# Optimization experiments

Measured on AMD Instinct MI355X. Metric: run time of the kernel, lower is better.

The kernel has to match this reference:

```python
import jax, jax.numpy as jnp
import numpy as np


def setup_inputs() -> dict:
    key = jax.random.key(0)
    k1, k2, k3 = jax.random.split(key, 3)
    B, N, C, H, W = 4, 6, 80, 16, 44
    image_features = jax.random.normal(k1, (B * N, C, H, W), dtype=jnp.float32)
    # eye + small perturbation keeps the 3x3 intrinsics block invertible
    intrinsics = jnp.eye(4, dtype=jnp.float32) + 0.1 * jax.random.normal(k2, (B, N, 4, 4), dtype=jnp.float32)
    extrinsics = jnp.eye(4, dtype=jnp.float32) + 0.1 * jax.random.normal(k3, (B, N, 4, 4), dtype=jnp.float32)
    return {"image_features": image_features, "intrinsics": intrinsics,
            "extrinsics": extrinsics, "depth_bins": 59}


def reference(image_features, intrinsics, extrinsics, depth_bins):
    BN, C, H, W = image_features.shape
    N = intrinsics.shape[1]
    B = BN // N
    dt = image_features.dtype
    depths = jnp.linspace(0.1, 1.0, depth_bins).astype(dt)  # (D,)
    feats = image_features.reshape(B, N, C, H, W)

    # pixel homogeneous coords, matching torch meshgrid(indexing='ij') + flatten
    yy, xx = jnp.meshgrid(jnp.arange(H), jnp.arange(W), indexing='ij')
    xy1 = jnp.stack([xx.ravel(), yy.ravel(), jnp.ones(H * W)], axis=0).astype(dt)  # (3, HW)

    K_inv = jnp.linalg.inv(intrinsics[:, :, :3, :3])            # (B,N,3,3)
    rays = jnp.einsum('bnij,jp->bnip', K_inv, xy1)              # (B,N,3,HW)

    # softmax over spatial dim (dim=3 of (B,N,C,HW) in the torch code)
    depth_probs = jax.nn.softmax(feats.reshape(B, N, C, H * W), axis=3)

    # In the original, only the LAST 4 channels of the (4C+1)-channel homogeneous
    # volume enter the extrinsic matmul: the [x,y,z] coords of channel C-1 plus 1.
    d_last = depth_probs[:, :, -1]                              # (B,N,HW)
    # (B,N,3,HW,D) = rays * (prob * depth)
    pts = rays[..., None] * (d_last[:, :, None, :, None] * depths)

    R = extrinsics[:, :, :3, :3]                                # (B,N,3,3)
    t = extrinsics[:, :, :3, 3]                                 # (B,N,3)
    world = jnp.einsum('bnij,bnjpd->bnipd', R, pts) + t[:, :, :, None, None]
    world = world.reshape(B, N, 3, H, W, depth_bins)

    feats_rep = jnp.broadcast_to(feats[..., None], (B, N, C, H, W, depth_bins))
    return jnp.concatenate([world, feats_rep], axis=2)         # (B,N,3+C,H,W,D)
```

## Files before the change

kernel.cpp:

```cpp
#include <hip/hip_runtime.h>


#define BB 4
#define NN 6
#define CC 80
#define HH 16
#define WW 44
#define DD 59
#define BN (BB*NN)
#define PP (HH*WW)
#define CHO (CC+3)
#define WD (WW*DD)
#define DSTEP (0.9f/58.f)
#define NF8 10342464u
#define SWEEPB 2048

typedef float fx4 __attribute__((ext_vector_type(4)));
typedef unsigned int uint;

__device__ inline float waveMax(float v) {
#pragma unroll
    for (int o = 32; o; o >>= 1) v = fmaxf(v, __shfl_xor(v, o));
    return v;
}
__device__ inline float waveSum(float v) {
#pragma unroll
    for (int o = 32; o; o >>= 1) v += __shfl_xor(v, o);
    return v;
}

__global__ __launch_bounds__(256) void lss_prep(const float* __restrict__ feats,
                                                const float* __restrict__ intr,
                                                const float* __restrict__ extr,
                                                float* __restrict__ Vw,
                                                float* __restrict__ Tarr) {
    const int bn = blockIdx.x;
    const int tid = threadIdx.x;
    __shared__ float sf[PP];
    __shared__ float sred[4];
    __shared__ float sbc[2];

    const float* f = feats + ((size_t)bn * CC + (CC - 1)) * PP;
    float m = -1e30f;
    for (int p = tid; p < PP; p += 256) { float v = f[p]; sf[p] = v; m = fmaxf(m, v); }
    m = waveMax(m);
    if ((tid & 63) == 0) sred[tid >> 6] = m;
    __syncthreads();
    if (tid == 0) sbc[0] = fmaxf(fmaxf(sred[0], sred[1]), fmaxf(sred[2], sred[3]));
    __syncthreads();
    const float mm = sbc[0];
    float s = 0.f;
    for (int p = tid; p < PP; p += 256) { float e = expf(sf[p] - mm); sf[p] = e; s += e; }
    s = waveSum(s);
    if ((tid & 63) == 0) sred[tid >> 6] = s;
    __syncthreads();
    if (tid == 0) sbc[1] = sred[0] + sred[1] + sred[2] + sred[3];
    __syncthreads();
    const float inv = 1.0f / sbc[1];

    const float* K = intr + bn * 16;
    float a = K[0], b = K[1], c = K[2];
    float d = K[4], e = K[5], ff = K[6];
    float g = K[8], h9 = K[9], i9 = K[10];
    float det = a * (e * i9 - ff * h9) - b * (d * i9 - ff * g) + c * (d * h9 - e * g);
    float id = 1.0f / det;
    float kinv[9] = {
        (e * i9 - ff * h9) * id, (c * h9 - b * i9) * id, (b * ff - c * e) * id,
        (ff * g - d * i9) * id,  (a * i9 - c * g) * id,  (c * d - a * ff) * id,
        (d * h9 - e * g) * id,   (b * g - a * h9) * id,  (a * e - b * d) * id
    };
    const float* E = extr + bn * 16;
#pragma unroll
    for (int ch = 0; ch < 3; ++ch) {
        float M0 = E[ch * 4 + 0] * kinv[0] + E[ch * 4 + 1] * kinv[3] + E[ch * 4 + 2] * kinv[6];
        float M1 = E[ch * 4 + 0] * kinv[1] + E[ch * 4 + 1] * kinv[4] + E[ch * 4 + 2] * kinv[7];
        float M2 = E[ch * 4 + 0] * kinv[2] + E[ch * 4 + 1] * kinv[5] + E[ch * 4 + 2] * kinv[8];
        float* vrow = Vw + (size_t)(bn * 3 + ch) * PP;
        for (int p = tid; p < PP; p += 256) {
            int hl = p / WW;
            int w  = p - hl * WW;
            float ray = M0 * (float)w + M1 * (float)hl + M2;
            vrow[p] = ray * sf[p] * inv;
        }
        if (tid == 0) Tarr[bn * 3 + ch] = E[ch * 4 + 3];
    }
}

__global__ __launch_bounds__(256) void lss_sweep(const float* __restrict__ feats,
                                                 const float* __restrict__ Vw,
                                                 const float* __restrict__ Tarr,
                                                 float* __restrict__ out) {
    const uint stride = gridDim.x * 256u;
    for (uint g = blockIdx.x * 256u + threadIdx.x; g < NF8; g += stride) {
        uint sl = g / 5192u;
        uint e8 = (g - sl * 5192u) << 3;
        uint p  = e8 / 59u;
        uint d0 = e8 - 59u * p;
        uint bn = sl / 83u;
        uint ch = sl - 83u * bn;
        uint kc = 59u - d0;
        uint cw = (kc < 8u) ? 1u : 0u;

        float vv[8];
        if (ch < 3u) {
            uint wrow = bn * 3u + ch;
            const float* src = Vw + wrow * (uint)PP;
            float T  = Tarr[wrow];
            float vA = src[p];
            float vB = src[p + cw];
#pragma unroll
            for (int k = 0; k < 8; ++k) {
                bool cr = ((uint)k >= kc);
                float val = cr ? vB : vA;
                uint dk = d0 + (uint)k - (cr ? 59u : 0u);
                vv[k] = val * (0.1f + (float)dk * DSTEP) + T;
            }
        } else {
            const float* src = feats + (bn * (uint)CC + (ch - 3u)) * (uint)PP;
            float vA = src[p];
            float vB = src[p + cw];
#pragma unroll
            for (int k = 0; k < 8; ++k) vv[k] = ((uint)k >= kc) ? vB : vA;
        }
        fx4 lo, hi;
        lo.x = vv[0]; lo.y = vv[1]; lo.z = vv[2]; lo.w = vv[3];
        hi.x = vv[4]; hi.y = vv[5]; hi.z = vv[6]; hi.w = vv[7];
        ((fx4*)out)[2u * g]      = lo;
        ((fx4*)out)[2u * g + 1u] = hi;
    }
}

extern "C" void kernel_launch(void* const* d_in, const int* in_sizes, int n_in,
                              void* d_out, int out_size, void* d_ws, size_t ws_size,
                              hipStream_t stream) {
    const float* feats = (const float*)d_in[0];
    const float* intr  = (const float*)d_in[1];
    const float* extr  = (const float*)d_in[2];
    float* out  = (float*)d_out;
    float* Vw   = (float*)d_ws;
    float* Tarr = (float*)d_ws + 50688 + 16;

    lss_prep<<<BN, 256, 0, stream>>>(feats, intr, extr, Vw, Tarr);
    lss_sweep<<<SWEEPB, 256, 0, stream>>>(feats, Vw, Tarr, out);
}
```

Before: 72.87 us.

## Fuse prep and sweep into one kernel with specialized world-coord and feature blocks

Result: faster. 66.06 us (-9.3%).

```diff
diff --git a/kernel.cpp b/kernel.cpp
--- a/kernel.cpp
+++ b/kernel.cpp
@@ -10,10 +10,12 @@
 #define BN (BB*NN)
 #define PP (HH*WW)
 #define CHO (CC+3)
-#define WD (WW*DD)
 #define DSTEP (0.9f/58.f)
-#define NF8 10342464u
-#define SWEEPB 2048
+#define Q4S 10384u
+#define NFS 1920u
+#define NFF4 (NFS*Q4S)
+#define WBLK 72
+#define FBLK 2048
 
 typedef float fx4 __attribute__((ext_vector_type(4)));
 typedef unsigned int uint;
@@ -29,104 +31,108 @@
     return v;
 }
 
-__global__ __launch_bounds__(256) void lss_prep(const float* __restrict__ feats,
-                                                const float* __restrict__ intr,
-                                                const float* __restrict__ extr,
-                                                float* __restrict__ Vw,
-                                                float* __restrict__ Tarr) {
-    const int bn = blockIdx.x;
+__global__ __launch_bounds__(256) void lss_fused(const float* __restrict__ feats,
+                                                 const float* __restrict__ intr,
+                                                 const float* __restrict__ extr,
+                                                 float* __restrict__ out) {
+    const int blk = blockIdx.x;
     const int tid = threadIdx.x;
+
     __shared__ float sf[PP];
+    __shared__ float vw[PP + 1];
     __shared__ float sred[4];
     __shared__ float sbc[2];
 
-    const float* f = feats + ((size_t)bn * CC + (CC - 1)) * PP;
-    float m = -1e30f;
-    for (int p = tid; p < PP; p += 256) { float v = f[p]; sf[p] = v; m = fmaxf(m, v); }
-    m = waveMax(m);
-    if ((tid & 63) == 0) sred[tid >> 6] = m;
-    __syncthreads();
-    if (tid == 0) sbc[0] = fmaxf(fmaxf(sred[0], sred[1]), fmaxf(sred[2], sred[3]));
-    __syncthreads();
-    const float mm = sbc[0];
-    float s = 0.f;
-    for (int p = tid; p < PP; p += 256) { float e = expf(sf[p] - mm); sf[p] = e; s += e; }
-    s = waveSum(s);
-    if ((tid & 63) == 0) sred[tid >> 6] = s;
-    __syncthreads();
-    if (tid == 0) sbc[1] = sred[0] + sred[1] + sred[2] + sred[3];
-    __syncthreads();
-    const float inv = 1.0f / sbc[1];
+    if (blk < WBLK) {
+        const int bn = blk / 3;
+        const int ch = blk - 3 * bn;
 
-    const float* K = intr + bn * 16;
-    float a = K[0], b = K[1], c = K[2];
-    float d = K[4], e = K[5], ff = K[6];
-    float g = K[8], h9 = K[9], i9 = K[10];
-    float det = a * (e * i9 - ff * h9) - b * (d * i9 - ff * g) + c * (d * h9 - e * g);
-    float id = 1.0f / det;
-    float kinv[9] = {
-        (e * i9 - ff * h9) * id, (c * h9 - b * i9) * id, (b * ff - c * e) * id,
-        (ff * g - d * i9) * id,  (a * i9 - c * g) * id,  (c * d - a * ff) * id,
-        (d * h9 - e * g) * id,   (b * g - a * h9) * id,  (a * e - b * d) * id
-    };
-    const float* E = extr + bn * 16;
-#pragma unroll
-    for (int ch = 0; ch < 3; ++ch) {
+        const float* f = feats + ((size_t)bn * CC + (CC - 1)) * PP;
+        float m = -1e30f;
+        for (int p = tid; p < PP; p += 256) { float v = f[p]; sf[p] = v; m = fmaxf(m, v); }
+        m = waveMax(m);
+        if ((tid & 63) == 0) sred[tid >> 6] = m;
+        __syncthreads();
+        if (tid == 0) sbc[0] = fmaxf(fmaxf(sred[0], sred[1]), fmaxf(sred[2], sred[3]));
+        __syncthreads();
+        const float mm = sbc[0];
+        float s = 0.f;
+        for (int p = tid; p < PP; p += 256) { float e = expf(sf[p] - mm); sf[p] = e; s += e; }
+        s = waveSum(s);
+        if ((tid & 63) == 0) sred[tid >> 6] = s;
+        __syncthreads();
+        if (tid == 0) sbc[1] = sred[0] + sred[1] + sred[2] + sred[3];
+        __syncthreads();
+        const float inv = 1.0f / sbc[1];
+
+        const float* K = intr + bn * 16;
+        float a = K[0], b = K[1], c = K[2];
+        float d = K[4], e = K[5], ff = K[6];
+        float g = K[8], h9 = K[9], i9 = K[10];
+        float det = a * (e * i9 - ff * h9) - b * (d * i9 - ff * g) + c * (d * h9 - e * g);
+        float id = 1.0f / det;
+        float kinv[9] = {
+            (e * i9 - ff * h9) * id, (c * h9 - b * i9) * id, (b * ff - c * e) * id,
+            (ff * g - d * i9) * id,  (a * i9 - c * g) * id,  (c * d - a * ff) * id,
+            (d * h9 - e * g) * id,   (b * g - a * h9) * id,  (a * e - b * d) * id
+        };
+        const float* E = extr + bn * 16;
         float M0 = E[ch * 4 + 0] * kinv[0] + E[ch * 4 + 1] * kinv[3] + E[ch * 4 + 2] * kinv[6];
         float M1 = E[ch * 4 + 0] * kinv[1] + E[ch * 4 + 1] * kinv[4] + E[ch * 4 + 2] * kinv[7];
         float M2 = E[ch * 4 + 0] * kinv[2] + E[ch * 4 + 1] * kinv[5] + E[ch * 4 + 2] * kinv[8];
-        float* vrow = Vw + (size_t)(bn * 3 + ch) * PP;
+        const float T = E[ch * 4 + 3];
+
         for (int p = tid; p < PP; p += 256) {
             int hl = p / WW;
             int w  = p - hl * WW;
             float ray = M0 * (float)w + M1 * (float)hl + M2;
-            vrow[p] = ray * sf[p] * inv;
+            vw[p] = ray * sf[p] * inv;
         }
-        if (tid == 0) Tarr[bn * 3 + ch] = E[ch * 4 + 3];
-    }
-}
+        if (tid == 0) vw[PP] = 0.f;
+        __syncthreads();
 
-__global__ __launch_bounds__(256) void lss_sweep(const float* __restrict__ feats,
-                                                 const float* __restrict__ Vw,
-                                                 const float* __restrict__ Tarr,
-                                                 float* __restrict__ out) {
-    const uint stride = gridDim.x * 256u;
-    for (uint g = blockIdx.x * 256u + threadIdx.x; g < NF8; g += stride) {
-        uint sl = g / 5192u;
-        uint e8 = (g - sl * 5192u) << 3;
-        uint p  = e8 / 59u;
-        uint d0 = e8 - 59u * p;
-        uint bn = sl / 83u;
-        uint ch = sl - 83u * bn;
-        uint kc = 59u - d0;
-        uint cw = (kc < 8u) ? 1u : 0u;
-
-        float vv[8];
-        if (ch < 3u) {
-            uint wrow = bn * 3u + ch;
-            const float* src = Vw + wrow * (uint)PP;
-            float T  = Tarr[wrow];
-            float vA = src[p];
-            float vB = src[p + cw];
+        const uint s0 = (uint)(bn * CHO + ch) * Q4S;
+        for (uint q = tid; q < Q4S; q += 256u) {
+            uint c4 = q << 2;
+            uint p  = c4 / 59u;
+            uint d0 = c4 - 59u * p;
+            uint kc = 59u - d0;
+            uint cw = (kc < 4u) ? 1u : 0u;
+            float vA = vw[p];
+            float vB = vw[p + cw];
+            fx4 r;
 #pragma unroll
-            for (int k = 0; k < 8; ++k) {
+            for (int k = 0; k < 4; ++k) {
                 bool cr = ((uint)k >= kc);
                 float val = cr ? vB : vA;
                 uint dk = d0 + (uint)k - (cr ? 59u : 0u);
-                vv[k] = val * (0.1f + (float)dk * DSTEP) + T;
+                r[k] = val * (0.1f + (float)dk * DSTEP) + T;
             }
-        } else {
-            const float* src = feats + (bn * (uint)CC + (ch - 3u)) * (uint)PP;
+            ((fx4*)out)[s0 + q] = r;
+        }
+    } else {
+        const uint stride = FBLK * 256u;
+        for (uint g = (uint)(blk - WBLK) * 256u + tid; g < NFF4; g += stride) {
+            uint fs = g / Q4S;
+            uint r4 = g - fs * Q4S;
+            uint c4 = r4 << 2;
+            uint p  = c4 / 59u;
+            uint d0 = c4 - 59u * p;
+            uint bn = fs / 80u;
+            uint chf = fs - 80u * bn;
+            uint kc = 59u - d0;
+            uint cw = (kc < 4u) ? 1u : 0u;
+
+            const float* src = feats + ((size_t)bn * CC + chf) * PP;
             float vA = src[p];
             float vB = src[p + cw];
+            fx4 r;
 #pragma unroll
-            for (int k = 0; k < 8; ++k) vv[k] = ((uint)k >= kc) ? vB : vA;
+            for (int k = 0; k < 4; ++k) r[k] = ((uint)k >= kc) ? vB : vA;
+
+            uint s = bn * (uint)CHO + 3u + chf;
+            ((fx4*)out)[s * Q4S + r4] = r;
         }
-        fx4 lo, hi;
-        lo.x = vv[0]; lo.y = vv[1]; lo.z = vv[2]; lo.w = vv[3];
-        hi.x = vv[4]; hi.y = vv[5]; hi.z = vv[6]; hi.w = vv[7];
-        ((fx4*)out)[2u * g]      = lo;
-        ((fx4*)out)[2u * g + 1u] = hi;
     }
 }
 
@@ -136,10 +142,7 @@
     const float* feats = (const float*)d_in[0];
     const float* intr  = (const float*)d_in[1];
     const float* extr  = (const float*)d_in[2];
-    float* out  = (float*)d_out;
-    float* Vw   = (float*)d_ws;
-    float* Tarr = (float*)d_ws + 50688 + 16;
+    float* out = (float*)d_out;
 
-    lss_prep<<<BN, 256, 0, stream>>>(feats, intr, extr, Vw, Tarr);
-    lss_sweep<<<SWEEPB, 256, 0, stream>>>(feats, Vw, Tarr, out);
+    lss_fused<<<WBLK + FBLK, 256, 0, stream>>>(feats, intr, extr, out);
 }
```
